# Kernel tuning notes

Hardware: AMD Instinct MI355X
Metric: run time of the kernel (lower is better)

## Reference

```python
import jax, jax.numpy as jnp
import numpy as np


def _generate_anchors(anc, grid):
    # anc: (A,2) = (w,h); grid: (B,H,W,2) = (x,y) centers
    # -> anchors (B,A,H,W,4) = (x_tl, y_tl, x_br, y_br)
    centers = jnp.concatenate([grid, grid], axis=-1)[:, None, :, :, :]  # (B,1,H,W,4)
    half = 0.5 * jnp.stack([-anc[:, 0], -anc[:, 1], anc[:, 0], anc[:, 1]], axis=-1)  # (A,4)
    return centers + half[None, :, None, None, :]


def _generate_proposals_yolo(anchors, offsets):
    # anchors, offsets: (B,A,H,W,4) -> proposals (B,A,H,W,4)
    x_ca = 0.5 * (anchors[..., 0] + anchors[..., 2])
    y_ca = 0.5 * (anchors[..., 1] + anchors[..., 3])
    wa = anchors[..., 2] - anchors[..., 0]
    ha = anchors[..., 3] - anchors[..., 1]
    # YOLO transform: center shift is additive, size is log-space scale
    x_cp = x_ca + offsets[..., 0]
    y_cp = y_ca + offsets[..., 1]
    wp = wa * jnp.exp(offsets[..., 2])
    hp = ha * jnp.exp(offsets[..., 3])
    return jnp.stack([x_cp - 0.5 * wp, y_cp - 0.5 * hp,
                      x_cp + 0.5 * wp, y_cp + 0.5 * hp], axis=-1)


def _iou(proposals, bboxes):
    # proposals: (B,A,H,W,4); bboxes: (B,N,5) -> iou_mat (B, A*H*W, N)
    B = proposals.shape[0]
    p = proposals.reshape(B, -1, 1, 4)          # (B, AHW, 1, 4)
    b = bboxes[:, None, :, :4]                   # (B, 1,  N, 4)
    tl = jnp.maximum(p[..., :2], b[..., :2])     # (B, AHW, N, 2)
    br = jnp.minimum(p[..., 2:], b[..., 2:])
    no_inter = (tl[..., 0] > br[..., 0]) | (tl[..., 1] > br[..., 1])
    aoi = (br[..., 0] - tl[..., 0]) * (br[..., 1] - tl[..., 1])
    aoi = jnp.where(no_inter, 0.0, aoi)
    aop = (p[..., 2] - p[..., 0]) * (p[..., 3] - p[..., 1])  # (B, AHW, 1)
    aob = (b[..., 2] - b[..., 0]) * (b[..., 3] - b[..., 1])  # (B, 1,  N)
    return aoi / (aop + aob - aoi)


def setup_inputs() -> dict:
    key = jax.random.key(0)
    k1, k2, k3, k4 = jax.random.split(key, 4)
    B, A, H, W, N = 16, 9, 56, 56, 64
    anc = jax.random.uniform(k1, (A, 2), dtype=jnp.float32)          # anchor (w,h) shapes
    grid = jax.random.uniform(k2, (B, H, W, 2), dtype=jnp.float32)   # cell centers
    offsets = jax.random.normal(k3, (B, A, H, W, 4), dtype=jnp.float32)
    bboxes = jax.random.uniform(k4, (B, N, 5), dtype=jnp.float32)    # GT boxes (x1,y1,x2,y2,cls)
    return {"anc": anc, "grid": grid, "offsets": offsets, "bboxes": bboxes}


def reference(anc, grid, offsets, bboxes):
    anchors = _generate_anchors(anc, grid)
    proposals = _generate_proposals_yolo(anchors, offsets)
    iou_mat = _iou(proposals, bboxes)
    return iou_mat
```

## Files before the change

kernel.cpp:

```cpp
#include <hip/hip_runtime.h>
#include <hip/hip_bf16.h>


constexpr int B_ = 16;
constexpr int A_ = 9;
constexpr int H_ = 56;
constexpr int W_ = 56;
constexpr int N_ = 64;
constexpr int HW_ = H_ * W_;
constexpr int P_ = A_ * HW_;
constexpr int WPB = P_ / 64;
constexpr int NWAVES = B_ * WPB;
constexpr int BLOCK = 256;

typedef float floatx4 __attribute__((ext_vector_type(4)));

__global__ __launch_bounds__(BLOCK) void ssd_iou_kernel(
    const float* __restrict__ anc,
    const float* __restrict__ grid,
    const float* __restrict__ offsets,
    const float* __restrict__ bboxes,
    float* __restrict__ out)
{
    const int t    = blockIdx.x * BLOCK + threadIdx.x;
    const int w    = t >> 6;
    const int lane = t & 63;

    const int b  = w / WPB;
    const int lp = (w - b * WPB) * 64 + lane;

    const int a  = lp / HW_;
    const int hw = lp - a * HW_;

    const float4 off = reinterpret_cast<const float4*>(offsets)[b * P_ + lp];
    const float2 g   = reinterpret_cast<const float2*>(grid)[b * HW_ + hw];
    const float  aw  = anc[2 * a + 0];
    const float  ah  = anc[2 * a + 1];

    const float xc = g.x + off.x;
    const float yc = g.y + off.y;
    const float wp = aw * __expf(off.z);
    const float hp = ah * __expf(off.w);

    const float mx0 = xc - 0.5f * wp;
    const float my0 = yc - 0.5f * hp;
    const float mx1 = xc + 0.5f * wp;
    const float my1 = yc + 0.5f * hp;

    const int q   = lane >> 4;
    const int g16 = lane & 15;

    float bx0[4], by0[4], bx1[4], by1[4], aob[4];
    #pragma unroll
    for (int k = 0; k < 4; ++k) {
        const float* bb = bboxes + ((size_t)(b * N_ + 4 * g16 + k)) * 5;
        bx0[k] = bb[0];
        by0[k] = bb[1];
        bx1[k] = bb[2];
        by1[k] = bb[3];
        aob[k] = (bx1[k] - bx0[k]) * (by1[k] - by0[k]);
    }

    float* obase = out + (size_t)w * (64 * N_) + q * N_ + 4 * g16;

    #pragma unroll
    for (int j = 0; j < 16; ++j) {
        const int src = 4 * j + q;
        const float px0 = __shfl(mx0, src);
        const float py0 = __shfl(my0, src);
        const float px1 = __shfl(mx1, src);
        const float py1 = __shfl(my1, src);
        const float aop = (px1 - px0) * (py1 - py0);

        floatx4 res;
        #pragma unroll
        for (int k = 0; k < 4; ++k) {
            const float tlx = fmaxf(px0, bx0[k]);
            const float tly = fmaxf(py0, by0[k]);
            const float brx = fminf(px1, bx1[k]);
            const float bry = fminf(py1, by1[k]);

            const float iw  = fmaxf(brx - tlx, 0.0f);
            const float ih  = fmaxf(bry - tly, 0.0f);
            const float aoi = iw * ih;

            const float denom = aop + aob[k] - aoi;
            res[k] = aoi * __builtin_amdgcn_rcpf(denom);
        }

        *reinterpret_cast<floatx4*>(obase + (size_t)j * (4 * N_)) = res;
    }
}

extern "C" void kernel_launch(void* const* d_in, const int* in_sizes, int n_in,
                              void* d_out, int out_size, void* d_ws, size_t ws_size,
                              hipStream_t stream) {
    const float* anc     = (const float*)d_in[0];
    const float* grid    = (const float*)d_in[1];
    const float* offsets = (const float*)d_in[2];
    const float* bboxes  = (const float*)d_in[3];
    float* out = (float*)d_out;

    const int nblocks = (NWAVES * 64) / BLOCK;
    ssd_iou_kernel<<<nblocks, BLOCK, 0, stream>>>(anc, grid, offsets, bboxes, out);
}
```

Measured before the change: 130.6 us.

## Remap waves to handle four proposals across all batches with vectorized bbox loads

```diff
diff --git a/kernel.cpp b/kernel.cpp
--- a/kernel.cpp
+++ b/kernel.cpp
@@ -9,13 +9,13 @@
 constexpr int N_ = 64;
 constexpr int HW_ = H_ * W_;
 constexpr int P_ = A_ * HW_;
-constexpr int WPB = P_ / 64;
-constexpr int NWAVES = B_ * WPB;
+constexpr int NSLOTS = P_ / 4;
 constexpr int BLOCK = 256;
+constexpr int NBLOCKS = NSLOTS * 64 / BLOCK;
 
 typedef float floatx4 __attribute__((ext_vector_type(4)));
 
-__global__ __launch_bounds__(BLOCK) void ssd_iou_kernel(
+__global__ __launch_bounds__(BLOCK, 7) void ssd_iou_kernel(
     const float* __restrict__ anc,
     const float* __restrict__ grid,
     const float* __restrict__ offsets,
@@ -23,17 +23,16 @@
     float* __restrict__ out)
 {
     const int t    = blockIdx.x * BLOCK + threadIdx.x;
-    const int w    = t >> 6;
+    const int s    = t >> 6;
     const int lane = t & 63;
 
-    const int b  = w / WPB;
-    const int lp = (w - b * WPB) * 64 + lane;
-
+    const int bl = lane >> 2;
+    const int lp = 4 * s + (lane & 3);
     const int a  = lp / HW_;
     const int hw = lp - a * HW_;
 
-    const float4 off = reinterpret_cast<const float4*>(offsets)[b * P_ + lp];
-    const float2 g   = reinterpret_cast<const float2*>(grid)[b * HW_ + hw];
+    const float4 off = reinterpret_cast<const float4*>(offsets)[bl * P_ + lp];
+    const float2 g   = reinterpret_cast<const float2*>(grid)[bl * HW_ + hw];
     const float  aw  = anc[2 * a + 0];
     const float  ah  = anc[2 * a + 1];
 
@@ -50,21 +49,22 @@
     const int q   = lane >> 4;
     const int g16 = lane & 15;
 
-    float bx0[4], by0[4], bx1[4], by1[4], aob[4];
-    #pragma unroll
-    for (int k = 0; k < 4; ++k) {
-        const float* bb = bboxes + ((size_t)(b * N_ + 4 * g16 + k)) * 5;
-        bx0[k] = bb[0];
-        by0[k] = bb[1];
-        bx1[k] = bb[2];
-        by1[k] = bb[3];
-        aob[k] = (bx1[k] - bx0[k]) * (by1[k] - by0[k]);
-    }
+    float* obase = out + (size_t)s * 256 + q * 64 + 4 * g16;
 
-    float* obase = out + (size_t)w * (64 * N_) + q * N_ + 4 * g16;
+    #pragma unroll 4
+    for (int j = 0; j < B_; ++j) {
+        const float4* bp =
+            reinterpret_cast<const float4*>(bboxes + j * (N_ * 5) + 20 * g16);
+        const float4 w0 = bp[0];
+        const float4 w1 = bp[1];
+        const float4 w2 = bp[2];
+        const float4 w3 = bp[3];
+        const float4 w4 = bp[4];
+        const float bx0[4] = { w0.x, w1.y, w2.z, w3.w };
+        const float by0[4] = { w0.y, w1.z, w2.w, w4.x };
+        const float bx1[4] = { w0.z, w1.w, w3.x, w4.y };
+        const float by1[4] = { w0.w, w2.x, w3.y, w4.z };
 
-    #pragma unroll
-    for (int j = 0; j < 16; ++j) {
         const int src = 4 * j + q;
         const float px0 = __shfl(mx0, src);
         const float py0 = __shfl(my0, src);
@@ -84,11 +84,12 @@
             const float ih  = fmaxf(bry - tly, 0.0f);
             const float aoi = iw * ih;
 
-            const float denom = aop + aob[k] - aoi;
+            const float aob   = (bx1[k] - bx0[k]) * (by1[k] - by0[k]);
+            const float denom = aop + aob - aoi;
             res[k] = aoi * __builtin_amdgcn_rcpf(denom);
         }
 
-        *reinterpret_cast<floatx4*>(obase + (size_t)j * (4 * N_)) = res;
+        *reinterpret_cast<floatx4*>(obase + (size_t)j * (NSLOTS * 256)) = res;
     }
 }
 
@@ -101,6 +102,5 @@
     const float* bboxes  = (const float*)d_in[3];
     float* out = (float*)d_out;
 
-    const int nblocks = (NWAVES * 64) / BLOCK;
-    ssd_iou_kernel<<<nblocks, BLOCK, 0, stream>>>(anc, grid, offsets, bboxes, out);
+    ssd_iou_kernel<<<NBLOCKS, BLOCK, 0, stream>>>(anc, grid, offsets, bboxes, out);
 }
```

Result: slower. 141.1 us (+8.1%).
